# Optimization experiments

Measured on AMD Instinct MI355X. Metric: run time of the kernel, lower is better.

Reference implementation:

```python
import jax, jax.numpy as jnp
import numpy as np
from jax import lax

T, C_IN, H0, W0 = 15, 6, 160, 160
C1, C2 = 128, 256
K1, K2 = 5, 2
THR1, THR2 = 10.0, 1.0
KWTA, RAD = 8, 1
W_MEAN, W_STD = 0.8, 0.05


def setup_inputs() -> dict:
    key = jax.random.key(0)
    k1, k2, k3 = jax.random.split(key, 3)
    # cumulative binary spike wave: each input neuron fires at a random time (or never)
    t_fire = jax.random.randint(k1, (C_IN, H0, W0), 0, 2 * T)
    inp = (jnp.arange(T)[:, None, None, None] >= t_fire[None]).astype(jnp.float32)
    w1 = W_MEAN + W_STD * jax.random.normal(k2, (C1, C_IN, K1, K1), jnp.float32)
    w2 = W_MEAN + W_STD * jax.random.normal(k3, (C2, C1, K2, K2), jnp.float32)
    return {"inp": inp, "w1": w1, "w2": w2, "layer_idx": 2}


def _conv(x, w):
    # x: [T, C, H, W] (time acts as batch), VALID conv, no bias (SpykeTorch snn.Convolution)
    return lax.conv_general_dilated(x, w, (1, 1), 'VALID',
                                    dimension_numbers=('NCHW', 'OIHW', 'NCHW'))


def _pad(x, p):
    return jnp.pad(x, ((0, 0), (0, 0), (p, p), (p, p)))


def _pool(x):
    # sf.pooling(s, 2, 2, 1): max-pool kernel 2, stride 2, padding 1 per time step
    return lax.reduce_window(x, -jnp.inf, lax.max,
                             (1, 1, 2, 2), (1, 1, 2, 2),
                             ((0, 0), (0, 0), (1, 1), (1, 1)))


def _fire(v, thr):
    # sf.fire with return_thresholded_potentials=True: zero out sub-threshold potentials
    v = jnp.where(v < thr, 0.0, v)
    return jnp.sign(v), v


def _pointwise_inhibition(v):
    # v: [T, C, H, W] nonneg.  At each spatial position, the feature with the max
    t, c = v.shape[0], v.shape[1]
    max_vals = v.max(axis=1)                      # [T,H,W]
    max_idx = v.argmax(axis=1).astype(jnp.int32)  # [T,H,W] winner channel per time
    clamp = jnp.sign(max_vals)                    # [T,H,W] any-spike indicator
    earliest = jnp.clip(t - clamp.sum(axis=0).astype(jnp.int32), 0, t - 1)  # [H,W]
    winner = jnp.take_along_axis(max_idx, earliest[None], axis=0)[0]        # [H,W]
    alive = clamp[-1]                             # [H,W] 1 if any spike ever
    coef = (jnp.arange(c)[:, None, None] == winner[None]).astype(v.dtype) * alive
    return v * coef[None]


def _get_k_winners(v, s, kwta, rad):
    # Greedy k-WTA with per-feature and spatial (radius) inhibition (NMS-like).
    t, c, h, w = v.shape
    earliest = jnp.clip(t - s.sum(axis=0).astype(jnp.int32), 0, t - 1)  # [C,H,W]
    vals = jnp.take_along_axis(v, earliest[None], axis=0)[0]            # potential at first spike
    trunc = s * vals
    big = trunc.max() * t                                               # earlier-spike dominance term
    trunc = trunc + s * big
    total = trunc.sum(axis=0)                                           # [C,H,W]

    ch_ids = jnp.arange(c)
    row_ids = jnp.arange(h)
    col_ids = jnp.arange(w)

    def step(total, _):
        idx = jnp.argmax(total.reshape(-1))
        mv = total.reshape(-1)[idx]
        f = (idx // (h * w)).astype(jnp.int32)
        rem = idx % (h * w)
        r = (rem // w).astype(jnp.int32)
        col = (rem % w).astype(jnp.int32)
        active = mv != 0
        kill = ((ch_ids == f)[:, None, None]
                | ((jnp.abs(row_ids - r) <= rad)[:, None]
                   & (jnp.abs(col_ids - col) <= rad)[None, :])[None])
        new_total = jnp.where(active, jnp.where(kill, 0.0, total), total)
        winner = jnp.where(active, jnp.stack([f, r, col]), -1)
        return new_total, winner

    _, winners = lax.scan(step, total, None, length=kwta)
    return winners  # [kwta, 3] (feature,row,col), -1 rows = inactive


def reference(inp, w1, w2, layer_idx):
    # training path, layer_idx == 2 (deepest branch)
    x = _pad(inp, 2)                       # [T,6,164,164]
    v = _conv(x, w1)                       # [T,128,160,160]
    s, v = _fire(v, THR1)
    s_in = _pad(_pool(s), 1)               # [T,128,83,83]
    s_in = _pointwise_inhibition(s_in)
    v = _conv(s_in, w2)                    # [T,256,82,82]
    s, v = _fire(v, THR2)
    v = _pointwise_inhibition(v)
    s = jnp.sign(v)
    winners = _get_k_winners(v, s, KWTA, RAD)
    return s, v, winners
```

## Files before the change

kernel.cpp:

```cpp
#include <hip/hip_runtime.h>

#define T_ 15
#define CIN 6
#define H0 160
#define W0 160
#define C1_ 128
#define C2_ 256
#define HP 83
#define H2 82
#define NPIX (H0*W0)
#define NIN (CIN*NPIX)
#define NPOS (H2*H2)
#define NS (T_*C2_*NPOS)
#define THR1 10.0f
#define THR2 1.0f

__global__ __launch_bounds__(256) void k_mega(const float* __restrict__ inp,
                                              const float* __restrict__ w1,
                                              const float* __restrict__ w2,
                                              unsigned int* __restrict__ maskg,
                                              float* __restrict__ w1T,
                                              float* __restrict__ w2T,
                                              unsigned int* __restrict__ bigbits,
                                              uint4* __restrict__ fill_dst,
                                              size_t n16, int nfill) {
    __shared__ unsigned char tft[CIN * 20 * 20];
    __shared__ int cnt[16 * 256];
    int b = blockIdx.x;
    int tid = threadIdx.x;

    if (b < 100) {
        int ty0 = (b / 10) * 16, tx0 = (b % 10) * 16;
        for (int i = tid; i < CIN * 400; i += 256) {
            int ci = i / 400, rem = i % 400;
            int ly = rem / 20, lx = rem % 20;
            int y = ty0 + ly - 2, x = tx0 + lx - 2;
            unsigned char tv = 15;
            if ((unsigned)y < (unsigned)H0 && (unsigned)x < (unsigned)W0) {
                float c = 0.f;
                int base = ci * NPIX + y * W0 + x;
#pragma unroll
                for (int t = 0; t < T_; t++) c += inp[(size_t)t * NIN + base];
                tv = (unsigned char)(15 - (int)(c + 0.5f));
            }
            tft[i] = tv;
        }
        __syncthreads();

        int tyl = tid >> 4, txl = tid & 15;
        int pix = (ty0 + tyl) * W0 + (tx0 + txl);
        int* col = cnt + tid;

#pragma unroll
        for (int w = 0; w < 5; w++) {
            int j0 = w * 32, j1 = (w == 4) ? 150 : (j0 + 32);
#pragma unroll
            for (int q = 0; q < 16; q++) col[q * 256] = 0;
#pragma unroll 32
            for (int j = j0; j < j1; j++) {
                int ci = j / 25, r = j % 25, ky = r / 5, kx = r % 5;
                int tfv = tft[ci * 400 + (tyl + ky) * 20 + (txl + kx)];
                col[tfv * 256] |= 1u << (j & 31);
            }
#pragma unroll
            for (int t = 0; t < 15; t++)
                maskg[(size_t)(t * 5 + w) * NPIX + pix] = (unsigned)col[t * 256];
        }
    } else if (b < 175) {
        if (b == 100 && tid == 0) *bigbits = 0u;
        int idx = (b - 100) * 256 + tid;
        int j = idx >> 7, c = idx & 127;
        w1T[idx] = w1[c * 150 + j];
    } else if (b < 687) {
        int idx = (b - 175) * 256 + tid;
        int o = idx & 255, kcc = idx >> 8;
        int cc = kcc & 127, k = kcc >> 7;
        w2T[idx] = w2[o * 512 + cc * 4 + k];
    } else {
        size_t stride = (size_t)nfill * 256;
        uint4 z = make_uint4(0u, 0u, 0u, 0u);
        for (size_t i = (size_t)(b - 687) * 256 + tid; i < n16; i += stride)
            fill_dst[i] = z;
    }
}

__global__ __launch_bounds__(256) void k1_main(const unsigned int* __restrict__ maskg,
                                               const float* __restrict__ w1T,
                                               unsigned char* __restrict__ fst1) {
    int wid = blockIdx.x * 4 + (threadIdx.x >> 6);
    int lane = threadIdx.x & 63;
    const float* wb = w1T + 2 * lane;
    for (int pix = wid; pix < NPIX; pix += 6400) {
        float v0 = 0.f, v1 = 0.f;
        int f0 = 15, f1 = 15;
        for (int t = 0; t < 15; ++t) {
            float b0 = 0.f, b1 = 0.f;
#pragma unroll
            for (int w = 0; w < 5; ++w) {
                unsigned int m = maskg[(size_t)(t * 5 + w) * NPIX + pix];
                int base = w * 32;
                while (m) {
                    int j = base + __builtin_ctz(m);
                    m &= m - 1;
                    float2 ww = *(const float2*)(wb + j * C1_);
                    b0 += ww.x; b1 += ww.y;
                }
            }
            v0 += b0; v1 += b1;
            f0 = (f0 == 15 && v0 >= THR1) ? t : f0;
            f1 = (f1 == 15 && v1 >= THR1) ? t : f1;
            if (__all((f0 < 15) & (f1 < 15))) break;
        }
        *(uchar2*)(fst1 + (size_t)pix * C1_ + 2 * lane) =
            make_uchar2((unsigned char)f0, (unsigned char)f1);
    }
}

__global__ __launch_bounds__(256) void k2_pool(const unsigned char* __restrict__ fst1,
                                               unsigned char* __restrict__ win_t,
                                               unsigned char* __restrict__ win_ch) {
    int pos = blockIdx.x * 4 + (threadIdx.x >> 6);
    int lane = threadIdx.x & 63;
    if (pos >= HP * HP) return;
    int py = pos / HP, px = pos % HP;
    if (py == 0 || py == HP - 1 || px == 0 || px == HP - 1) {
        if (lane == 0) { win_t[pos] = 15; win_ch[pos] = 0; }
        return;
    }
    int y0 = 2 * py - 3, x0 = 2 * px - 3;
    int m0 = 15, m1 = 15;
#pragma unroll
    for (int dy = 0; dy < 2; dy++) {
        int y = y0 + dy;
        if ((unsigned)y < (unsigned)H0) {
#pragma unroll
            for (int dx = 0; dx < 2; dx++) {
                int x = x0 + dx;
                if ((unsigned)x < (unsigned)W0) {
                    uchar2 f = *(const uchar2*)(fst1 + (size_t)(y * W0 + x) * C1_ + 2 * lane);
                    m0 = f.x < m0 ? f.x : m0;
                    m1 = f.y < m1 ? f.y : m1;
                }
            }
        }
    }
    int k0 = (m0 << 8) | (2 * lane);
    int k1 = (m1 << 8) | (2 * lane + 1);
    int key = k0 < k1 ? k0 : k1;
#pragma unroll
    for (int off = 32; off > 0; off >>= 1) {
        int other = __shfl_xor(key, off);
        key = other < key ? other : key;
    }
    if (lane == 0) {
        win_t[pos] = (unsigned char)(key >> 8);
        win_ch[pos] = (unsigned char)(key & 255);
    }
}

__global__ __launch_bounds__(256) void kz_fill(uint4* __restrict__ dst, size_t n16,
                                               unsigned int* __restrict__ bigbits) {
    size_t stride = (size_t)gridDim.x * 256;
    uint4 z = make_uint4(0u, 0u, 0u, 0u);
    for (size_t i = (size_t)blockIdx.x * 256 + threadIdx.x; i < n16; i += stride)
        dst[i] = z;
    if (blockIdx.x == 0 && threadIdx.x == 0) *bigbits = 0u;
}

__global__ __launch_bounds__(256) void k3_conv2(const unsigned char* __restrict__ win_t,
                                                const unsigned char* __restrict__ win_ch,
                                                const float* __restrict__ w2T,
                                                float* __restrict__ s_out,
                                                float* __restrict__ v_out,
                                                float* __restrict__ vals,
                                                int* __restrict__ nsp_arr,
                                                int* __restrict__ ow_arr,
                                                unsigned int* __restrict__ bigbits) {
    __shared__ unsigned int ormask;
    __shared__ unsigned long long amax;
    int p = blockIdx.x;
    int y2 = p / H2, x2 = p % H2;
    int o = threadIdx.x;
    if (o == 0) { ormask = 0u; amax = 0ull; }
    __syncthreads();

    float w[4]; int tj[4];
#pragma unroll
    for (int k = 0; k < 4; k++) {
        int dy = k >> 1, dx = k & 1;
        int pi = (y2 + dy) * HP + (x2 + dx);
        int tt = win_t[pi];
        int cc = win_ch[pi];
        tj[k] = tt;
        w[k] = (tt < 15) ? w2T[(k * C1_ + cc) * 256 + o] : 0.0f;
    }

    float z[T_];
    unsigned int m = 0u;
#pragma unroll
    for (int t = 0; t < T_; t++) {
        float v = 0.f;
#pragma unroll
        for (int k = 0; k < 4; k++) v += (t >= tj[k]) ? w[k] : 0.f;
        float zz = (v < THR2) ? 0.f : v;
        z[t] = zz;
        m |= (zz > 0.f) ? (1u << t) : 0u;
    }

    unsigned int mw = m;
#pragma unroll
    for (int off = 32; off > 0; off >>= 1) mw |= __shfl_xor(mw, off);
    if ((o & 63) == 0) atomicOr(&ormask, mw);
    __syncthreads();

    unsigned int om = ormask;
    int count = __popc(om & 0x7FFFu);
    int earliest = 15 - count;
    earliest = earliest < 0 ? 0 : (earliest > 14 ? 14 : earliest);
    int alive = (om >> 14) & 1;

    float zval = 0.f;
#pragma unroll
    for (int t = 0; t < T_; t++) zval = (t == earliest) ? z[t] : zval;

    unsigned long long key =
        ((unsigned long long)__float_as_uint(zval) << 16) | (unsigned long long)(1023 - o);
#pragma unroll
    for (int off = 32; off > 0; off >>= 1) {
        unsigned long long other = __shfl_xor(key, off);
        key = other > key ? other : key;
    }
    if ((o & 63) == 0) atomicMax(&amax, key);
    __syncthreads();

    if (alive) {
        int wo = 1023 - (int)(amax & 0xFFFFull);
        if (o == wo) {
            int nsp = __popc(m & 0x7FFFu);
            int e2 = 15 - nsp;
            e2 = e2 < 0 ? 0 : (e2 > 14 ? 14 : e2);
            float vv = 0.f;
#pragma unroll
            for (int t = 0; t < T_; t++) vv = (t == e2) ? z[t] : vv;
            vals[p] = vv; nsp_arr[p] = nsp; ow_arr[p] = wo;
            if (nsp > 0) atomicMax(bigbits, __float_as_uint(vv));
#pragma unroll
            for (int t = 0; t < T_; t++) {
                if (z[t] != 0.f) {
                    int idx = ((t * C2_ + wo) * H2 + y2) * H2 + x2;
                    v_out[idx] = z[t];
                    s_out[idx] = 1.0f;
                }
            }
        }
    } else if (o == 0) {
        vals[p] = 0.f; nsp_arr[p] = 0; ow_arr[p] = 0;
    }
}

__global__ __launch_bounds__(1024) void k4_kwta(const float* __restrict__ vals,
                                                const int* __restrict__ nsp,
                                                const int* __restrict__ ow,
                                                const unsigned int* __restrict__ bigbits,
                                                float* __restrict__ wout) {
    __shared__ float tot[NPOS];
    __shared__ short och[NPOS];
    __shared__ unsigned long long amax;
    int tid = threadIdx.x;
    float big = __uint_as_float(*bigbits) * 15.0f;

    for (int p = tid; p < NPOS; p += 1024) {
        int n = nsp[p];
        tot[p] = (n > 0) ? (float)n * (vals[p] + big) : 0.0f;
        och[p] = (short)ow[p];
    }
    if (tid == 0) amax = 0ull;
    __syncthreads();

    for (int it = 0; it < 8; it++) {
        unsigned long long best = 0ull;
        for (int p = tid; p < NPOS; p += 1024) {
            float tv = tot[p];
            if (tv > 0.0f) {
                unsigned int k = (unsigned)och[p] * (unsigned)NPOS + (unsigned)p;
                unsigned long long pk =
                    ((unsigned long long)__float_as_uint(tv) << 21) |
                    (unsigned long long)(0x1FFFFFu - k);
                best = pk > best ? pk : best;
            }
        }
#pragma unroll
        for (int off = 32; off > 0; off >>= 1) {
            unsigned long long other = __shfl_xor(best, off);
            best = other > best ? other : best;
        }
        if ((tid & 63) == 0) atomicMax(&amax, best);
        __syncthreads();
        unsigned long long mx = amax;
        __syncthreads();
        if (tid == 0) amax = 0ull;

        if (mx == 0ull) {
            if (tid == 0) {
                wout[it * 3 + 0] = -1.f; wout[it * 3 + 1] = -1.f; wout[it * 3 + 2] = -1.f;
            }
        } else {
            unsigned int k = 0x1FFFFFu - (unsigned)(mx & 0x1FFFFFull);
            int f = (int)(k / NPOS), pp = (int)(k % NPOS);
            int r = pp / H2, col = pp % H2;
            if (tid == 0) {
                wout[it * 3 + 0] = (float)f; wout[it * 3 + 1] = (float)r; wout[it * 3 + 2] = (float)col;
            }
            for (int p = tid; p < NPOS; p += 1024) {
                int pr = p / H2, pc = p % H2;
                bool kill = (och[p] == (short)f) ||
                            (pr >= r - 1 && pr <= r + 1 && pc >= col - 1 && pc <= col + 1);
                if (kill) tot[p] = 0.0f;
            }
        }
        __syncthreads();
    }
}

extern "C" void kernel_launch(void* const* d_in, const int* in_sizes, int n_in,
                              void* d_out, int out_size, void* d_ws, size_t ws_size,
                              hipStream_t stream) {
    const float* inp = (const float*)d_in[0];
    const float* w1  = (const float*)d_in[1];
    const float* w2  = (const float*)d_in[2];

    float* out = (float*)d_out;
    float* s_out = out;
    float* v_out = out + (size_t)NS;
    float* wnr   = out + 2 * (size_t)NS;

    size_t need = (size_t)15 << 20;
    bool big_ws = ws_size >= need;
    char* scratch = big_ws ? (char*)d_ws
                           : (char*)d_out + (size_t)NS * sizeof(float);
    unsigned int* maskg = (unsigned int*)scratch;
    unsigned char* fst1 = (unsigned char*)(scratch + (8 << 20));
    float* w1T = (float*)(scratch + (12 << 20));
    float* w2T = (float*)(scratch + (13 << 20));
    char* smol = big_ws ? (char*)d_ws + (14 << 20) : (char*)d_ws;
    unsigned char* win_t  = (unsigned char*)smol;
    unsigned char* win_ch = (unsigned char*)smol + 8192;
    float* vals = (float*)(smol + 16384);
    int*   nsp  = (int*)(smol + 49152);
    int*   ow   = (int*)(smol + 81920);
    unsigned int* bigbits = (unsigned int*)(smol + 114688);

    size_t n16 = (size_t)out_size / 4;
    int nfill = big_ws ? 4096 : 0;

    hipLaunchKernelGGL(k_mega, dim3(687 + nfill), dim3(256), 0, stream,
                       inp, w1, w2, maskg, w1T, w2T, bigbits, (uint4*)d_out, n16, nfill);
    hipLaunchKernelGGL(k1_main, dim3(1600), dim3(256), 0, stream, maskg, w1T, fst1);
    hipLaunchKernelGGL(k2_pool, dim3((HP * HP + 3) / 4), dim3(256), 0, stream,
                       fst1, win_t, win_ch);
    if (!big_ws)
        hipLaunchKernelGGL(kz_fill, dim3(4096), dim3(256), 0, stream,
                           (uint4*)d_out, n16, bigbits);
    hipLaunchKernelGGL(k3_conv2, dim3(NPOS), dim3(256), 0, stream,
                       win_t, win_ch, w2T, s_out, v_out, vals, nsp, ow, bigbits);
    hipLaunchKernelGGL(k4_kwta, dim3(1), dim3(1024), 0, stream, vals, nsp, ow, bigbits, wnr);
}
```

Baseline: 207.2 us.

## Split output zero-fill across kernels and map one wavefront per conv2 position

Splits the output zero-fill into two halves. The first half runs in extra blocks of the prep kernel and the second half in extra blocks of the layer-1 kernel, so the memory-bound fill overlaps with compute in both. The layer-1 kernel now uses one pixel per wave with no grid-stride loop. Conv2 goes from one 256-thread block per position to one wavefront per position, with each lane covering 4 output channels. This removes shared-memory atomics and __syncthreads, and the potentials are recomputed from the winner's weights instead of kept in a 15-element array. The cost is more registers per lane and some redundant arithmetic.

```diff
diff --git a/kernel.cpp b/kernel.cpp
--- a/kernel.cpp
+++ b/kernel.cpp
@@ -14,6 +14,8 @@
 #define NS (T_*C2_*NPOS)
 #define THR1 10.0f
 #define THR2 1.0f
+#define NF1 2048
+#define NF2 2048
 
 __global__ __launch_bounds__(256) void k_mega(const float* __restrict__ inp,
                                               const float* __restrict__ w1,
@@ -23,7 +25,7 @@
                                               float* __restrict__ w2T,
                                               unsigned int* __restrict__ bigbits,
                                               uint4* __restrict__ fill_dst,
-                                              size_t n16, int nfill) {
+                                              size_t nA, int nf) {
     __shared__ unsigned char tft[CIN * 20 * 20];
     __shared__ int cnt[16 * 256];
     int b = blockIdx.x;
@@ -77,43 +79,53 @@
         int cc = kcc & 127, k = kcc >> 7;
         w2T[idx] = w2[o * 512 + cc * 4 + k];
     } else {
-        size_t stride = (size_t)nfill * 256;
+        size_t stride = (size_t)nf * 256;
         uint4 z = make_uint4(0u, 0u, 0u, 0u);
-        for (size_t i = (size_t)(b - 687) * 256 + tid; i < n16; i += stride)
+        for (size_t i = (size_t)(b - 687) * 256 + tid; i < nA; i += stride)
             fill_dst[i] = z;
     }
 }
 
 __global__ __launch_bounds__(256) void k1_main(const unsigned int* __restrict__ maskg,
                                                const float* __restrict__ w1T,
-                                               unsigned char* __restrict__ fst1) {
-    int wid = blockIdx.x * 4 + (threadIdx.x >> 6);
-    int lane = threadIdx.x & 63;
+                                               unsigned char* __restrict__ fst1,
+                                               uint4* __restrict__ fill_dst,
+                                               size_t nA, size_t n16, int nf) {
+    int b = blockIdx.x;
+    int tid = threadIdx.x;
+    if (b >= 6400) {
+        size_t stride = (size_t)nf * 256;
+        uint4 z = make_uint4(0u, 0u, 0u, 0u);
+        for (size_t i = nA + (size_t)(b - 6400) * 256 + tid; i < n16; i += stride)
+            fill_dst[i] = z;
+        return;
+    }
+    int pix = b * 4 + (tid >> 6);
+    int lane = tid & 63;
     const float* wb = w1T + 2 * lane;
-    for (int pix = wid; pix < NPIX; pix += 6400) {
-        float v0 = 0.f, v1 = 0.f;
-        int f0 = 15, f1 = 15;
-        for (int t = 0; t < 15; ++t) {
-            float b0 = 0.f, b1 = 0.f;
-#pragma unroll
-            for (int w = 0; w < 5; ++w) {
-                unsigned int m = maskg[(size_t)(t * 5 + w) * NPIX + pix];
-                int base = w * 32;
-                while (m) {
-                    int j = base + __builtin_ctz(m);
-                    m &= m - 1;
-                    float2 ww = *(const float2*)(wb + j * C1_);
-                    b0 += ww.x; b1 += ww.y;
-                }
-            }
-            v0 += b0; v1 += b1;
-            f0 = (f0 == 15 && v0 >= THR1) ? t : f0;
-            f1 = (f1 == 15 && v1 >= THR1) ? t : f1;
-            if (__all((f0 < 15) & (f1 < 15))) break;
-        }
-        *(uchar2*)(fst1 + (size_t)pix * C1_ + 2 * lane) =
-            make_uchar2((unsigned char)f0, (unsigned char)f1);
-    }
+
+    float v0 = 0.f, v1 = 0.f;
+    int f0 = 15, f1 = 15;
+    for (int t = 0; t < 15; ++t) {
+        float b0 = 0.f, b1 = 0.f;
+#pragma unroll
+        for (int w = 0; w < 5; ++w) {
+            unsigned int m = maskg[(size_t)(t * 5 + w) * NPIX + pix];
+            int base = w * 32;
+            while (m) {
+                int j = base + __builtin_ctz(m);
+                m &= m - 1;
+                float2 ww = *(const float2*)(wb + j * C1_);
+                b0 += ww.x; b1 += ww.y;
+            }
+        }
+        v0 += b0; v1 += b1;
+        f0 = (f0 == 15 && v0 >= THR1) ? t : f0;
+        f1 = (f1 == 15 && v1 >= THR1) ? t : f1;
+        if (__all((f0 < 15) & (f1 < 15))) break;
+    }
+    *(uchar2*)(fst1 + (size_t)pix * C1_ + 2 * lane) =
+        make_uchar2((unsigned char)f0, (unsigned char)f1);
 }
 
 __global__ __launch_bounds__(256) void k2_pool(const unsigned char* __restrict__ fst1,
@@ -176,84 +188,104 @@
                                                 int* __restrict__ nsp_arr,
                                                 int* __restrict__ ow_arr,
                                                 unsigned int* __restrict__ bigbits) {
-    __shared__ unsigned int ormask;
-    __shared__ unsigned long long amax;
-    int p = blockIdx.x;
+    int p = blockIdx.x * 4 + (threadIdx.x >> 6);
+    int lane = threadIdx.x & 63;
     int y2 = p / H2, x2 = p % H2;
-    int o = threadIdx.x;
-    if (o == 0) { ormask = 0u; amax = 0ull; }
-    __syncthreads();
-
-    float w[4]; int tj[4];
+
+    int tj[4]; int ccv[4];
 #pragma unroll
     for (int k = 0; k < 4; k++) {
         int dy = k >> 1, dx = k & 1;
         int pi = (y2 + dy) * HP + (x2 + dx);
-        int tt = win_t[pi];
-        int cc = win_ch[pi];
-        tj[k] = tt;
-        w[k] = (tt < 15) ? w2T[(k * C1_ + cc) * 256 + o] : 0.0f;
-    }
-
-    float z[T_];
-    unsigned int m = 0u;
-#pragma unroll
-    for (int t = 0; t < T_; t++) {
-        float v = 0.f;
-#pragma unroll
-        for (int k = 0; k < 4; k++) v += (t >= tj[k]) ? w[k] : 0.f;
-        float zz = (v < THR2) ? 0.f : v;
-        z[t] = zz;
-        m |= (zz > 0.f) ? (1u << t) : 0u;
-    }
-
-    unsigned int mw = m;
-#pragma unroll
-    for (int off = 32; off > 0; off >>= 1) mw |= __shfl_xor(mw, off);
-    if ((o & 63) == 0) atomicOr(&ormask, mw);
-    __syncthreads();
-
-    unsigned int om = ormask;
+        tj[k] = win_t[pi];
+        ccv[k] = win_ch[pi];
+    }
+
+    float wq[4][4];
+    unsigned int mq[4];
+    unsigned int lane_or = 0u;
+#pragma unroll
+    for (int q = 0; q < 4; q++) {
+        int ch = q * 64 + lane;
+#pragma unroll
+        for (int k = 0; k < 4; k++)
+            wq[q][k] = (tj[k] < 15) ? w2T[(k * C1_ + ccv[k]) * 256 + ch] : 0.0f;
+        unsigned int m = 0u;
+#pragma unroll
+        for (int t = 0; t < T_; t++) {
+            float v = 0.f;
+#pragma unroll
+            for (int k = 0; k < 4; k++) v += (t >= tj[k]) ? wq[q][k] : 0.f;
+            m |= (v >= THR2) ? (1u << t) : 0u;
+        }
+        mq[q] = m;
+        lane_or |= m;
+    }
+
+#pragma unroll
+    for (int off = 32; off > 0; off >>= 1) lane_or |= __shfl_xor(lane_or, off);
+    unsigned int om = lane_or;
     int count = __popc(om & 0x7FFFu);
     int earliest = 15 - count;
     earliest = earliest < 0 ? 0 : (earliest > 14 ? 14 : earliest);
     int alive = (om >> 14) & 1;
 
-    float zval = 0.f;
-#pragma unroll
-    for (int t = 0; t < T_; t++) zval = (t == earliest) ? z[t] : zval;
-
-    unsigned long long key =
-        ((unsigned long long)__float_as_uint(zval) << 16) | (unsigned long long)(1023 - o);
+    unsigned long long best = 0ull;
+    float bw0 = 0.f, bw1 = 0.f, bw2 = 0.f, bw3 = 0.f;
+    unsigned int bm = 0u;
+#pragma unroll
+    for (int q = 0; q < 4; q++) {
+        int ch = q * 64 + lane;
+        float v = 0.f;
+#pragma unroll
+        for (int k = 0; k < 4; k++) v += (earliest >= tj[k]) ? wq[q][k] : 0.f;
+        float zval = (v < THR2) ? 0.f : v;
+        unsigned long long key =
+            ((unsigned long long)__float_as_uint(zval) << 16) |
+            (unsigned long long)(1023 - ch);
+        if (key > best) {
+            best = key;
+            bw0 = wq[q][0]; bw1 = wq[q][1]; bw2 = wq[q][2]; bw3 = wq[q][3];
+            bm = mq[q];
+        }
+    }
+    unsigned long long gbest = best;
 #pragma unroll
     for (int off = 32; off > 0; off >>= 1) {
-        unsigned long long other = __shfl_xor(key, off);
-        key = other > key ? other : key;
-    }
-    if ((o & 63) == 0) atomicMax(&amax, key);
-    __syncthreads();
+        unsigned long long other = __shfl_xor(gbest, off);
+        gbest = other > gbest ? other : gbest;
+    }
 
     if (alive) {
-        int wo = 1023 - (int)(amax & 0xFFFFull);
-        if (o == wo) {
-            int nsp = __popc(m & 0x7FFFu);
+        int wo = 1023 - (int)(gbest & 0xFFFFull);
+        if ((wo & 63) == lane && best == gbest) {
+            int nsp = __popc(bm & 0x7FFFu);
             int e2 = 15 - nsp;
             e2 = e2 < 0 ? 0 : (e2 > 14 ? 14 : e2);
             float vv = 0.f;
 #pragma unroll
-            for (int t = 0; t < T_; t++) vv = (t == e2) ? z[t] : vv;
+            for (int k = 0; k < 4; k++) {
+                float wk = (k == 0) ? bw0 : (k == 1) ? bw1 : (k == 2) ? bw2 : bw3;
+                vv += (e2 >= tj[k]) ? wk : 0.f;
+            }
+            vv = (vv < THR2) ? 0.f : vv;
             vals[p] = vv; nsp_arr[p] = nsp; ow_arr[p] = wo;
             if (nsp > 0) atomicMax(bigbits, __float_as_uint(vv));
 #pragma unroll
             for (int t = 0; t < T_; t++) {
-                if (z[t] != 0.f) {
+                if ((bm >> t) & 1u) {
+                    float vt = 0.f;
+                    vt += (t >= tj[0]) ? bw0 : 0.f;
+                    vt += (t >= tj[1]) ? bw1 : 0.f;
+                    vt += (t >= tj[2]) ? bw2 : 0.f;
+                    vt += (t >= tj[3]) ? bw3 : 0.f;
                     int idx = ((t * C2_ + wo) * H2 + y2) * H2 + x2;
-                    v_out[idx] = z[t];
+                    v_out[idx] = vt;
                     s_out[idx] = 1.0f;
                 }
             }
         }
-    } else if (o == 0) {
+    } else if (lane == 0) {
         vals[p] = 0.f; nsp_arr[p] = 0; ow_arr[p] = 0;
     }
 }
@@ -351,17 +383,20 @@
     unsigned int* bigbits = (unsigned int*)(smol + 114688);
 
     size_t n16 = (size_t)out_size / 4;
-    int nfill = big_ws ? 4096 : 0;
-
-    hipLaunchKernelGGL(k_mega, dim3(687 + nfill), dim3(256), 0, stream,
-                       inp, w1, w2, maskg, w1T, w2T, bigbits, (uint4*)d_out, n16, nfill);
-    hipLaunchKernelGGL(k1_main, dim3(1600), dim3(256), 0, stream, maskg, w1T, fst1);
+    size_t nA  = big_ws ? n16 / 2 : 0;
+    int nf1 = big_ws ? NF1 : 0;
+    int nf2 = big_ws ? NF2 : 0;
+
+    hipLaunchKernelGGL(k_mega, dim3(687 + nf1), dim3(256), 0, stream,
+                       inp, w1, w2, maskg, w1T, w2T, bigbits, (uint4*)d_out, nA, nf1);
+    hipLaunchKernelGGL(k1_main, dim3(6400 + nf2), dim3(256), 0, stream,
+                       maskg, w1T, fst1, (uint4*)d_out, nA, n16, nf2);
     hipLaunchKernelGGL(k2_pool, dim3((HP * HP + 3) / 4), dim3(256), 0, stream,
                        fst1, win_t, win_ch);
     if (!big_ws)
         hipLaunchKernelGGL(kz_fill, dim3(4096), dim3(256), 0, stream,
                            (uint4*)d_out, n16, bigbits);
-    hipLaunchKernelGGL(k3_conv2, dim3(NPOS), dim3(256), 0, stream,
+    hipLaunchKernelGGL(k3_conv2, dim3(NPOS / 4), dim3(256), 0, stream,
                        win_t, win_ch, w2T, s_out, v_out, vals, nsp, ow, bigbits);
     hipLaunchKernelGGL(k4_kwta, dim3(1), dim3(1024), 0, stream, vals, nsp, ow, bigbits, wnr);
 }
```

Result: faster. 199.6 us (-3.7%).
